# Kernel optimization log

Measured on AMD Instinct MI355X. Metric: run time of the kernel, lower is better.

The kernel has to match this reference:

```python
import jax, jax.numpy as jnp
import numpy as np

N, M, D = 100000, 50000, 256
NE = N + M
B = 131072

def kl_normal_std(mu, scale):
    # KL( N(mu, scale) || N(0, 1) ) = -log(scale) + (scale^2 + mu^2)/2 - 1/2
    return 0.5 * (scale * scale + mu * mu - 1.0) - jnp.log(scale)

def setup_inputs() -> dict:
    key = jax.random.key(0)
    ks = jax.random.split(key, 8)
    users = jax.random.randint(ks[0], (B, 1), 0, N)
    items = jax.random.randint(ks[1], (B, 1), N, NE)
    x = jnp.concatenate([users, items], axis=1)                        # [B, 2]
    bias_table = jax.random.normal(ks[2], (NE, 2), dtype=jnp.float32)
    entity_table = jax.random.normal(ks[3], (NE, 2 * D), dtype=jnp.float32)
    global_bias_mean = jnp.zeros((1,), dtype=jnp.float32)
    global_bias_scale = jnp.ones((1,), dtype=jnp.float32)
    nb_occ = jax.random.randint(ks[4], (NE,), 1, 1001)                 # train occurrence counts >= 1
    eps_bias = jax.random.normal(ks[5], (NE,), dtype=jnp.float32)
    eps_entity = jax.random.normal(ks[6], (NE, D), dtype=jnp.float32)
    eps_global = jax.random.normal(ks[7], (1,), dtype=jnp.float32)
    return {"x": x, "bias_table": bias_table, "entity_table": entity_table,
            "global_bias_mean": global_bias_mean, "global_bias_scale": global_bias_scale,
            "nb_occ": nb_occ, "eps_bias": eps_bias, "eps_entity": eps_entity,
            "eps_global": eps_global}

def reference(x, bias_table, entity_table, global_bias_mean, global_bias_scale,
              nb_occ, eps_bias, eps_entity, eps_global):
    # --- reparameterized samples (one eps per table row == one eps per unique entity) ---
    gb_scale = jnp.abs(global_bias_scale)
    global_bias = global_bias_mean + gb_scale * eps_global             # [1]

    bias_mu = bias_table[:, 0]
    bias_sc = jnp.abs(bias_table[:, 1])
    biases_all = bias_mu + bias_sc * eps_bias                          # [NE]

    ent_mu = entity_table[:, :D]
    ent_sc = jnp.abs(entity_table[:, D:])
    entities_all = ent_mu + ent_sc * eps_entity                        # [NE, D]

    # --- FM forward: bias sum + product-sum interaction ---
    pair_bias = biases_all[x].sum(axis=1)                              # [B]
    pair_emb = (entities_all[x[:, 0]] * entities_all[x[:, 1]]).sum(axis=1)  # [B]
    logits = global_bias + pair_bias + pair_emb                        # [B] (Bernoulli logits)

    # --- closed-form KL vs N(0,1), rescaled by batch/train occupancy ---
    kl_bias = kl_normal_std(bias_mu, bias_sc)                          # [NE]
    kl_entity = kl_normal_std(ent_mu, ent_sc).sum(axis=1)              # [NE]

    nb_occ_f = nb_occ.astype(jnp.float32)
    cnt = jnp.bincount(x.reshape(-1), length=NE).astype(jnp.float32)   # nb_occ_in_batch
    cnt_u = jnp.bincount(x[:, 0], length=NE).astype(jnp.float32)
    cnt_i = jnp.bincount(x[:, 1], length=NE).astype(jnp.float32)
    user_norm = (cnt_u / nb_occ_f).sum()
    item_norm = (cnt_i / nb_occ_f).sum()

    ids = jnp.arange(NE)
    scale_term = (jnp.where(ids <= N, float(N), 0.0) / user_norm
                  + jnp.where(ids > N, float(M), 0.0) / item_norm)
    kl_rescaled = ((kl_bias + kl_entity) * (cnt / nb_occ_f) * scale_term).sum()

    kl_global = kl_normal_std(global_bias_mean, gb_scale).sum()
    return logits, kl_global + kl_rescaled
```

## Files before the change

### kernel.cpp

```cpp
#include <hip/hip_runtime.h>
#include <math.h>

#define NU   100000
#define MI   50000
#define NEn  150000
#define Bp   131072

#define CB   256
#define EB   (NEn / 4)
#define TB   ((NEn + 255) / 256)
#define LB   (Bp / 8)

typedef float    f4v __attribute__((ext_vector_type(4)));
typedef _Float16 h8v __attribute__((ext_vector_type(8)));
typedef _Float16 h4v __attribute__((ext_vector_type(4)));

__device__ __forceinline__ float wred(float v) {
#pragma unroll
    for (int m = 32; m > 0; m >>= 1) v += __shfl_xor(v, m, 64);
    return v;
}
__device__ __forceinline__ float hred(float v) {
#pragma unroll
    for (int m = 16; m > 0; m >>= 1) v += __shfl_xor(v, m, 64);
    return v;
}

__global__ __launch_bounds__(256) void k_cnt_ent(
    const int4* __restrict__ x4,
    const f4v* __restrict__ et,
    const f4v* __restrict__ epse,
    const float* __restrict__ bt,
    const float* __restrict__ epsb,
    const float* __restrict__ gbm,
    const float* __restrict__ gbs,
    int*   __restrict__ cnt,
    h4v*   __restrict__ enth,
    float* __restrict__ bia,
    float* __restrict__ klpe,
    float* __restrict__ outkl)
{
    if (blockIdx.x < CB) {
        int t = blockIdx.x * 256 + threadIdx.x;
        int4 v = x4[t];
        atomicAdd(cnt + v.x, 1);
        atomicAdd(cnt + v.y, 1);
        atomicAdd(cnt + v.z, 1);
        atomicAdd(cnt + v.w, 1);
        if (t == 0) {
            float gm = gbm[0];
            float gs = fabsf(gbs[0]);
            outkl[0] = 0.5f * (gs * gs + gm * gm - 1.0f) - __logf(gs);
        }
        return;
    }

    int lane = threadIdx.x & 63;
    int e    = (blockIdx.x - CB) * 4 + (threadIdx.x >> 6);

    const f4v* row = et + (size_t)e * 128;
    f4v mu = __builtin_nontemporal_load(row + lane);
    f4v s4 = __builtin_nontemporal_load(row + 64 + lane);
    f4v ep = __builtin_nontemporal_load(epse + (size_t)e * 64 + lane);
    float scx = fabsf(s4.x), scy = fabsf(s4.y), scz = fabsf(s4.z), scw = fabsf(s4.w);

    if (enth) {
        h4v oh;
        oh.x = (_Float16)fmaf(scx, ep.x, mu.x);
        oh.y = (_Float16)fmaf(scy, ep.y, mu.y);
        oh.z = (_Float16)fmaf(scz, ep.z, mu.z);
        oh.w = (_Float16)fmaf(scw, ep.w, mu.w);
        enth[(size_t)e * 64 + lane] = oh;
    }

    float kl = 0.5f * (scx * scx + mu.x * mu.x - 1.0f) - __logf(scx)
             + 0.5f * (scy * scy + mu.y * mu.y - 1.0f) - __logf(scy)
             + 0.5f * (scz * scz + mu.z * mu.z - 1.0f) - __logf(scz)
             + 0.5f * (scw * scw + mu.w * mu.w - 1.0f) - __logf(scw);
    kl = wred(kl);

    if (lane == 0) {
        float bmu = bt[2 * e];
        float bsc = fabsf(bt[2 * e + 1]);
        bia[e]  = fmaf(bsc, epsb[e], bmu);
        klpe[e] = kl + 0.5f * (bsc * bsc + bmu * bmu - 1.0f) - __logf(bsc);
    }
}

__global__ __launch_bounds__(256) void k_log_tail(
    const int* __restrict__ x,
    const h8v* __restrict__ enth,
    const float* __restrict__ bia,
    const float* __restrict__ gbm, const float* __restrict__ gbs,
    const float* __restrict__ epsg,
    const int* __restrict__ cnt, const int* __restrict__ nb,
    const float* __restrict__ klpe,
    float* __restrict__ hdr,
    float* __restrict__ out)
{
    if (blockIdx.x < TB) {
        int e = blockIdx.x * 256 + threadIdx.x;
        float u = 0.f, i = 0.f, aa = 0.f, bb = 0.f;
        if (e < NEn) {
            float v  = (float)cnt[e] / (float)nb[e];
            float kv = klpe[e] * v;
            if (e < NU)  u  = v;  else i  = v;
            if (e <= NU) aa = kv; else bb = kv;
        }
        u = wred(u); i = wred(i); aa = wred(aa); bb = wred(bb);
        __shared__ float s[4][4];
        int wib = threadIdx.x >> 6;
        if ((threadIdx.x & 63) == 0) {
            s[wib][0] = u; s[wib][1] = i; s[wib][2] = aa; s[wib][3] = bb;
        }
        __syncthreads();
        if (threadIdx.x < 4) {
            float t = s[0][threadIdx.x] + s[1][threadIdx.x]
                    + s[2][threadIdx.x] + s[3][threadIdx.x];
            if (t != 0.f) atomicAdd(hdr + threadIdx.x, t);
        }
        return;
    }

    int lane = threadIdx.x & 63;
    int sub  = lane & 31;
    int p    = (blockIdx.x - TB) * 8 + ((threadIdx.x >> 6) << 1) + (lane >> 5);
    int u = x[2 * p], v = x[2 * p + 1];
    float bu = bia[u];
    float bv = bia[v];
    h8v a = enth[(size_t)u * 32 + sub];
    h8v b = enth[(size_t)v * 32 + sub];
    float d = 0.f;
#pragma unroll
    for (int i = 0; i < 8; ++i) d = fmaf((float)a[i], (float)b[i], d);
    d = hred(d);
    if (sub == 0) {
        float gb = fmaf(fabsf(gbs[0]), epsg[0], gbm[0]);
        __builtin_nontemporal_store(gb + bu + bv + d, out + p);
    }
}

__global__ void k_fin(const float* __restrict__ hdr, float* __restrict__ outkl) {
    if (threadIdx.x == 0)
        outkl[0] += (float)NU * hdr[2] / hdr[0] + (float)MI * hdr[3] / hdr[1];
}

__global__ __launch_bounds__(256) void k_logits_rc(
    const int* __restrict__ x, const float4* __restrict__ et,
    const float4* __restrict__ epse, const float* __restrict__ bia,
    const float* __restrict__ gbm, const float* __restrict__ gbs,
    const float* __restrict__ epsg, float* __restrict__ out)
{
    int lane = threadIdx.x & 63;
    int p    = blockIdx.x * 4 + (threadIdx.x >> 6);
    int u = x[2 * p], v = x[2 * p + 1];
    const float4* ru = et + (size_t)u * 128;
    const float4* rv = et + (size_t)v * 128;
    float4 mu_u = ru[lane], s_u = ru[64 + lane], e_u = epse[(size_t)u * 64 + lane];
    float4 mu_v = rv[lane], s_v = rv[64 + lane], e_v = epse[(size_t)v * 64 + lane];
    float ax = fmaf(fabsf(s_u.x), e_u.x, mu_u.x), bx = fmaf(fabsf(s_v.x), e_v.x, mu_v.x);
    float ay = fmaf(fabsf(s_u.y), e_u.y, mu_u.y), by = fmaf(fabsf(s_v.y), e_v.y, mu_v.y);
    float az = fmaf(fabsf(s_u.z), e_u.z, mu_u.z), bz = fmaf(fabsf(s_v.z), e_v.z, mu_v.z);
    float aw = fmaf(fabsf(s_u.w), e_u.w, mu_u.w), bw = fmaf(fabsf(s_v.w), e_v.w, mu_v.w);
    float d = ax * bx + ay * by + az * bz + aw * bw;
    d = wred(d);
    if (lane == 0) {
        float gb = fmaf(fabsf(gbs[0]), epsg[0], gbm[0]);
        out[p] = gb + bia[u] + bia[v] + d;
    }
}

extern "C" void kernel_launch(void* const* d_in, const int* in_sizes, int n_in,
                              void* d_out, int out_size, void* d_ws, size_t ws_size,
                              hipStream_t stream)
{
    const int*   x    = (const int*)d_in[0];
    const float* bt   = (const float*)d_in[1];
    const float* et   = (const float*)d_in[2];
    const float* gbm  = (const float*)d_in[3];
    const float* gbs  = (const float*)d_in[4];
    const int*   nb   = (const int*)d_in[5];
    const float* epsb = (const float*)d_in[6];
    const float* epse = (const float*)d_in[7];
    const float* epsg = (const float*)d_in[8];
    float* out = (float*)d_out;

    char*  ws   = (char*)d_ws;
    float* hdr  = (float*)ws;
    int*   cnt  = (int*)  (ws + 64);
    float* klpe = (float*)(ws + 64 + (size_t)NEn * 4);
    float* bia  = (float*)(ws + 64 + (size_t)NEn * 8);
    size_t entoff = 64 + (size_t)NEn * 12;
    h4v* enth = nullptr;
    if (ws_size >= entoff + (size_t)NEn * 512)
        enth = (h4v*)(ws + entoff);

    (void)hipMemsetAsync(ws, 0, 64 + (size_t)NEn * 4, stream);

    k_cnt_ent<<<CB + EB, 256, 0, stream>>>(
        (const int4*)x, (const f4v*)et, (const f4v*)epse, bt, epsb,
        gbm, gbs, cnt, enth, bia, klpe, out + Bp);

    if (enth) {
        k_log_tail<<<TB + LB, 256, 0, stream>>>(
            x, (const h8v*)enth, bia, gbm, gbs, epsg,
            cnt, nb, klpe, hdr, out);
    } else {
        k_log_tail<<<TB, 256, 0, stream>>>(
            x, nullptr, bia, gbm, gbs, epsg, cnt, nb, klpe, hdr, out);
        k_logits_rc<<<Bp / 4, 256, 0, stream>>>(x, (const float4*)et,
                                                (const float4*)epse, bia,
                                                gbm, gbs, epsg, out);
    }

    k_fin<<<1, 64, 0, stream>>>(hdr, out + Bp);
}
```

Before: 529.5 us.

## Replace bincount histogram with per-pair accumulation of KL weights in logits kernel

The atomic histogram pass and the memset of the count buffer are removed. Instead, the logits kernel accumulates klpe[e]/nb[e] and 1/nb[e] directly for each batch occurrence, which is algebraically the same as weighting each entity by its count. A special case sends the item index equal to N to the user-scaled sum. Both kernels become fixed-grid persistent loops, the entity kernel handles two rows per wave with vectorised bias loads, and block 0 zeroes the reduction header. The KL reduction now does scattered reads of nb and klpe per pair in exchange for dropping the histogram atomics and the separate per-entity tail pass.

```diff
diff --git a/kernel.cpp b/kernel.cpp
--- a/kernel.cpp
+++ b/kernel.cpp
@@ -6,12 +6,11 @@
 #define NEn  150000
 #define Bp   131072
 
-#define CB   256
-#define EB   (NEn / 4)
-#define TB   ((NEn + 255) / 256)
-#define LB   (Bp / 8)
+#define GRID1 2048
+#define GRID2 2048
 
 typedef float    f4v __attribute__((ext_vector_type(4)));
+typedef float    f2v __attribute__((ext_vector_type(2)));
 typedef _Float16 h8v __attribute__((ext_vector_type(8)));
 typedef _Float16 h4v __attribute__((ext_vector_type(4)));
 
@@ -26,117 +25,140 @@
     return v;
 }
 
-__global__ __launch_bounds__(256) void k_cnt_ent(
-    const int4* __restrict__ x4,
+__global__ __launch_bounds__(256) void k_ent(
     const f4v* __restrict__ et,
     const f4v* __restrict__ epse,
-    const float* __restrict__ bt,
-    const float* __restrict__ epsb,
+    const f2v* __restrict__ bt2,
+    const f2v* __restrict__ epsb2,
     const float* __restrict__ gbm,
     const float* __restrict__ gbs,
-    int*   __restrict__ cnt,
-    h4v*   __restrict__ enth,
-    float* __restrict__ bia,
-    float* __restrict__ klpe,
+    h4v*  __restrict__ enth,
+    f2v*  __restrict__ bia2,
+    f2v*  __restrict__ klpe2,
+    float* __restrict__ hdr,
     float* __restrict__ outkl)
 {
-    if (blockIdx.x < CB) {
-        int t = blockIdx.x * 256 + threadIdx.x;
-        int4 v = x4[t];
-        atomicAdd(cnt + v.x, 1);
-        atomicAdd(cnt + v.y, 1);
-        atomicAdd(cnt + v.z, 1);
-        atomicAdd(cnt + v.w, 1);
-        if (t == 0) {
-            float gm = gbm[0];
-            float gs = fabsf(gbs[0]);
+    if (blockIdx.x == 0) {
+        if (threadIdx.x < 4) hdr[threadIdx.x] = 0.f;
+        if (threadIdx.x == 0) {
+            float gm = gbm[0], gs = fabsf(gbs[0]);
             outkl[0] = 0.5f * (gs * gs + gm * gm - 1.0f) - __logf(gs);
         }
-        return;
-    }
-
-    int lane = threadIdx.x & 63;
-    int e    = (blockIdx.x - CB) * 4 + (threadIdx.x >> 6);
-
-    const f4v* row = et + (size_t)e * 128;
-    f4v mu = __builtin_nontemporal_load(row + lane);
-    f4v s4 = __builtin_nontemporal_load(row + 64 + lane);
-    f4v ep = __builtin_nontemporal_load(epse + (size_t)e * 64 + lane);
-    float scx = fabsf(s4.x), scy = fabsf(s4.y), scz = fabsf(s4.z), scw = fabsf(s4.w);
-
-    if (enth) {
-        h4v oh;
-        oh.x = (_Float16)fmaf(scx, ep.x, mu.x);
-        oh.y = (_Float16)fmaf(scy, ep.y, mu.y);
-        oh.z = (_Float16)fmaf(scz, ep.z, mu.z);
-        oh.w = (_Float16)fmaf(scw, ep.w, mu.w);
-        enth[(size_t)e * 64 + lane] = oh;
-    }
-
-    float kl = 0.5f * (scx * scx + mu.x * mu.x - 1.0f) - __logf(scx)
-             + 0.5f * (scy * scy + mu.y * mu.y - 1.0f) - __logf(scy)
-             + 0.5f * (scz * scz + mu.z * mu.z - 1.0f) - __logf(scz)
-             + 0.5f * (scw * scw + mu.w * mu.w - 1.0f) - __logf(scw);
-    kl = wred(kl);
-
-    if (lane == 0) {
-        float bmu = bt[2 * e];
-        float bsc = fabsf(bt[2 * e + 1]);
-        bia[e]  = fmaf(bsc, epsb[e], bmu);
-        klpe[e] = kl + 0.5f * (bsc * bsc + bmu * bmu - 1.0f) - __logf(bsc);
-    }
-}
-
-__global__ __launch_bounds__(256) void k_log_tail(
-    const int* __restrict__ x,
+    }
+
+    const int lane = threadIdx.x & 63;
+    const int gwav = blockIdx.x * 4 + (threadIdx.x >> 6);
+    const int step = GRID1 * 4 * 2;
+
+    for (int r0 = gwav * 2; r0 < NEn; r0 += step) {
+        const f4v* ra = et + (size_t)r0 * 128;
+        const f4v* rb = ra + 128;
+        f4v mu0 = __builtin_nontemporal_load(ra + lane);
+        f4v s40 = __builtin_nontemporal_load(ra + 64 + lane);
+        f4v mu1 = __builtin_nontemporal_load(rb + lane);
+        f4v s41 = __builtin_nontemporal_load(rb + 64 + lane);
+        f4v ep0 = __builtin_nontemporal_load(epse + (size_t)r0 * 64 + lane);
+        f4v ep1 = __builtin_nontemporal_load(epse + (size_t)r0 * 64 + 64 + lane);
+
+        float ax0 = fabsf(s40.x), ay0 = fabsf(s40.y), az0 = fabsf(s40.z), aw0 = fabsf(s40.w);
+        float ax1 = fabsf(s41.x), ay1 = fabsf(s41.y), az1 = fabsf(s41.z), aw1 = fabsf(s41.w);
+
+        if (enth) {
+            h4v o0, o1;
+            o0.x = (_Float16)fmaf(ax0, ep0.x, mu0.x);
+            o0.y = (_Float16)fmaf(ay0, ep0.y, mu0.y);
+            o0.z = (_Float16)fmaf(az0, ep0.z, mu0.z);
+            o0.w = (_Float16)fmaf(aw0, ep0.w, mu0.w);
+            o1.x = (_Float16)fmaf(ax1, ep1.x, mu1.x);
+            o1.y = (_Float16)fmaf(ay1, ep1.y, mu1.y);
+            o1.z = (_Float16)fmaf(az1, ep1.z, mu1.z);
+            o1.w = (_Float16)fmaf(aw1, ep1.w, mu1.w);
+            enth[(size_t)r0 * 64 + lane]      = o0;
+            enth[(size_t)r0 * 64 + 64 + lane] = o1;
+        }
+
+        float kl0 = 0.5f * (ax0 * ax0 + mu0.x * mu0.x - 1.0f) - __logf(ax0)
+                  + 0.5f * (ay0 * ay0 + mu0.y * mu0.y - 1.0f) - __logf(ay0)
+                  + 0.5f * (az0 * az0 + mu0.z * mu0.z - 1.0f) - __logf(az0)
+                  + 0.5f * (aw0 * aw0 + mu0.w * mu0.w - 1.0f) - __logf(aw0);
+        float kl1 = 0.5f * (ax1 * ax1 + mu1.x * mu1.x - 1.0f) - __logf(ax1)
+                  + 0.5f * (ay1 * ay1 + mu1.y * mu1.y - 1.0f) - __logf(ay1)
+                  + 0.5f * (az1 * az1 + mu1.z * mu1.z - 1.0f) - __logf(az1)
+                  + 0.5f * (aw1 * aw1 + mu1.w * mu1.w - 1.0f) - __logf(aw1);
+        kl0 = wred(kl0);
+        kl1 = wred(kl1);
+
+        if (lane == 0) {
+            f2v b0 = bt2[r0], b1 = bt2[r0 + 1];
+            f2v eb = epsb2[r0 >> 1];
+            float bs0 = fabsf(b0.y), bs1 = fabsf(b1.y);
+            f2v bo, ko;
+            bo.x = fmaf(bs0, eb.x, b0.x);
+            bo.y = fmaf(bs1, eb.y, b1.x);
+            ko.x = kl0 + 0.5f * (bs0 * bs0 + b0.x * b0.x - 1.0f) - __logf(bs0);
+            ko.y = kl1 + 0.5f * (bs1 * bs1 + b1.x * b1.x - 1.0f) - __logf(bs1);
+            bia2[r0 >> 1]  = bo;
+            klpe2[r0 >> 1] = ko;
+        }
+    }
+}
+
+__global__ __launch_bounds__(256) void k_log(
+    const int2* __restrict__ x2,
     const h8v* __restrict__ enth,
     const float* __restrict__ bia,
+    const float* __restrict__ klpe,
+    const int* __restrict__ nb,
     const float* __restrict__ gbm, const float* __restrict__ gbs,
     const float* __restrict__ epsg,
-    const int* __restrict__ cnt, const int* __restrict__ nb,
-    const float* __restrict__ klpe,
     float* __restrict__ hdr,
     float* __restrict__ out)
 {
-    if (blockIdx.x < TB) {
-        int e = blockIdx.x * 256 + threadIdx.x;
-        float u = 0.f, i = 0.f, aa = 0.f, bb = 0.f;
-        if (e < NEn) {
-            float v  = (float)cnt[e] / (float)nb[e];
-            float kv = klpe[e] * v;
-            if (e < NU)  u  = v;  else i  = v;
-            if (e <= NU) aa = kv; else bb = kv;
-        }
-        u = wred(u); i = wred(i); aa = wred(aa); bb = wred(bb);
-        __shared__ float s[4][4];
-        int wib = threadIdx.x >> 6;
-        if ((threadIdx.x & 63) == 0) {
-            s[wib][0] = u; s[wib][1] = i; s[wib][2] = aa; s[wib][3] = bb;
-        }
-        __syncthreads();
-        if (threadIdx.x < 4) {
-            float t = s[0][threadIdx.x] + s[1][threadIdx.x]
-                    + s[2][threadIdx.x] + s[3][threadIdx.x];
-            if (t != 0.f) atomicAdd(hdr + threadIdx.x, t);
-        }
-        return;
-    }
-
-    int lane = threadIdx.x & 63;
-    int sub  = lane & 31;
-    int p    = (blockIdx.x - TB) * 8 + ((threadIdx.x >> 6) << 1) + (lane >> 5);
-    int u = x[2 * p], v = x[2 * p + 1];
-    float bu = bia[u];
-    float bv = bia[v];
-    h8v a = enth[(size_t)u * 32 + sub];
-    h8v b = enth[(size_t)v * 32 + sub];
-    float d = 0.f;
+    const int lane = threadIdx.x & 63;
+    const int sub  = lane & 31;
+    const int grp  = (blockIdx.x * 4 + (threadIdx.x >> 6)) * 2 + (lane >> 5);
+    const int ngrp = GRID2 * 4 * 2;
+    const float gb = fmaf(fabsf(gbs[0]), epsg[0], gbm[0]);
+    const bool use_ent = (enth != nullptr);
+
+    float uS = 0.f, iS = 0.f, aS = 0.f, bS = 0.f;
+
+    for (int p = grp; p < Bp; p += ngrp) {
+        int2 pr = x2[p];
+        int u = pr.x, v = pr.y;
+        if (use_ent) {
+            float bu = bia[u];
+            float bv = bia[v];
+            h8v a = enth[(size_t)u * 32 + sub];
+            h8v b = enth[(size_t)v * 32 + sub];
+            float d = 0.f;
 #pragma unroll
-    for (int i = 0; i < 8; ++i) d = fmaf((float)a[i], (float)b[i], d);
-    d = hred(d);
-    if (sub == 0) {
-        float gb = fmaf(fabsf(gbs[0]), epsg[0], gbm[0]);
-        __builtin_nontemporal_store(gb + bu + bv + d, out + p);
+            for (int i = 0; i < 8; ++i) d = fmaf((float)a[i], (float)b[i], d);
+            d = hred(d);
+            if (sub == 0)
+                __builtin_nontemporal_store(gb + bu + bv + d, out + p);
+        }
+        if (sub == 0) {
+            float rnu = 1.0f / (float)nb[u];
+            float rnv = 1.0f / (float)nb[v];
+            float au  = klpe[u] * rnu;
+            float av  = klpe[v] * rnv;
+            uS += rnu;
+            iS += rnv;
+            aS += au + ((v == NU) ? av : 0.f);
+            bS += ((v > NU) ? av : 0.f);
+        }
+    }
+
+    uS = wred(uS); iS = wred(iS); aS = wred(aS); bS = wred(bS);
+    __shared__ float s[4][4];
+    int wib = threadIdx.x >> 6;
+    if (lane == 0) { s[wib][0] = uS; s[wib][1] = iS; s[wib][2] = aS; s[wib][3] = bS; }
+    __syncthreads();
+    if (threadIdx.x < 4) {
+        float t = s[0][threadIdx.x] + s[1][threadIdx.x]
+                + s[2][threadIdx.x] + s[3][threadIdx.x];
+        if (t != 0.f) atomicAdd(hdr + threadIdx.x, t);
     }
 }
 
@@ -187,31 +209,26 @@
 
     char*  ws   = (char*)d_ws;
     float* hdr  = (float*)ws;
-    int*   cnt  = (int*)  (ws + 64);
-    float* klpe = (float*)(ws + 64 + (size_t)NEn * 4);
-    float* bia  = (float*)(ws + 64 + (size_t)NEn * 8);
-    size_t entoff = 64 + (size_t)NEn * 12;
+    float* klpe = (float*)(ws + 64);
+    float* bia  = (float*)(ws + 64 + (size_t)NEn * 4);
+    size_t entoff = 64 + (size_t)NEn * 8;
     h4v* enth = nullptr;
     if (ws_size >= entoff + (size_t)NEn * 512)
         enth = (h4v*)(ws + entoff);
 
-    (void)hipMemsetAsync(ws, 0, 64 + (size_t)NEn * 4, stream);
-
-    k_cnt_ent<<<CB + EB, 256, 0, stream>>>(
-        (const int4*)x, (const f4v*)et, (const f4v*)epse, bt, epsb,
-        gbm, gbs, cnt, enth, bia, klpe, out + Bp);
-
-    if (enth) {
-        k_log_tail<<<TB + LB, 256, 0, stream>>>(
-            x, (const h8v*)enth, bia, gbm, gbs, epsg,
-            cnt, nb, klpe, hdr, out);
-    } else {
-        k_log_tail<<<TB, 256, 0, stream>>>(
-            x, nullptr, bia, gbm, gbs, epsg, cnt, nb, klpe, hdr, out);
+
+    k_ent<<<GRID1, 256, 0, stream>>>(
+        (const f4v*)et, (const f4v*)epse, (const f2v*)bt, (const f2v*)epsb,
+        gbm, gbs, enth, (f2v*)bia, (f2v*)klpe, hdr, out + Bp);
+
+    k_log<<<GRID2, 256, 0, stream>>>(
+        (const int2*)x, (const h8v*)enth, bia, klpe, nb,
+        gbm, gbs, epsg, hdr, out);
+
+    if (!enth)
         k_logits_rc<<<Bp / 4, 256, 0, stream>>>(x, (const float4*)et,
                                                 (const float4*)epse, bia,
                                                 gbm, gbs, epsg, out);
-    }
 
     k_fin<<<1, 64, 0, stream>>>(hdr, out + Bp);
 }
```

After: 554.0 us. 4.6% more time.

## Replace bincount histogram with per-pair KL accumulation and striped header atomics

Applied to the files above, without the earlier changes.

Drops the atomic histogram of entity occurrences and the per-entity tail reduction. The KL terms are now accumulated directly per pair inside the logits kernel, using the identity that a sum of cnt/nb over entities equals a sum of 1/nb over batch occurrences. This also removes the memset, since block 0 of the entity kernel zeroes the header. Header atomics are spread over 32 slots to reduce contention, and the final kernel sums them. The cost is extra random gathers of nb and klpe per pair, and a possible race because the header zeroing happens in the previous kernel.

```diff
diff --git a/kernel.cpp b/kernel.cpp
--- a/kernel.cpp
+++ b/kernel.cpp
@@ -6,11 +6,6 @@
 #define NEn  150000
 #define Bp   131072
 
-#define CB   256
-#define EB   (NEn / 4)
-#define TB   ((NEn + 255) / 256)
-#define LB   (Bp / 8)
-
 typedef float    f4v __attribute__((ext_vector_type(4)));
 typedef _Float16 h8v __attribute__((ext_vector_type(8)));
 typedef _Float16 h4v __attribute__((ext_vector_type(4)));
@@ -26,37 +21,29 @@
     return v;
 }
 
-__global__ __launch_bounds__(256) void k_cnt_ent(
-    const int4* __restrict__ x4,
+__global__ __launch_bounds__(256) void k_ent(
     const f4v* __restrict__ et,
     const f4v* __restrict__ epse,
     const float* __restrict__ bt,
     const float* __restrict__ epsb,
     const float* __restrict__ gbm,
     const float* __restrict__ gbs,
-    int*   __restrict__ cnt,
     h4v*   __restrict__ enth,
     float* __restrict__ bia,
     float* __restrict__ klpe,
+    float* __restrict__ hdr,
     float* __restrict__ outkl)
 {
-    if (blockIdx.x < CB) {
-        int t = blockIdx.x * 256 + threadIdx.x;
-        int4 v = x4[t];
-        atomicAdd(cnt + v.x, 1);
-        atomicAdd(cnt + v.y, 1);
-        atomicAdd(cnt + v.z, 1);
-        atomicAdd(cnt + v.w, 1);
-        if (t == 0) {
-            float gm = gbm[0];
-            float gs = fabsf(gbs[0]);
+    if (blockIdx.x == 0) {
+        if (threadIdx.x < 128) hdr[threadIdx.x] = 0.f;
+        if (threadIdx.x == 0) {
+            float gm = gbm[0], gs = fabsf(gbs[0]);
             outkl[0] = 0.5f * (gs * gs + gm * gm - 1.0f) - __logf(gs);
         }
-        return;
     }
 
     int lane = threadIdx.x & 63;
-    int e    = (blockIdx.x - CB) * 4 + (threadIdx.x >> 6);
+    int e    = blockIdx.x * 4 + (threadIdx.x >> 6);
 
     const f4v* row = et + (size_t)e * 128;
     f4v mu = __builtin_nontemporal_load(row + lane);
@@ -87,62 +74,76 @@
     }
 }
 
-__global__ __launch_bounds__(256) void k_log_tail(
-    const int* __restrict__ x,
+__global__ __launch_bounds__(256) void k_log(
+    const int2* __restrict__ x2,
     const h8v* __restrict__ enth,
     const float* __restrict__ bia,
+    const float* __restrict__ klpe,
+    const int* __restrict__ nb,
     const float* __restrict__ gbm, const float* __restrict__ gbs,
     const float* __restrict__ epsg,
-    const int* __restrict__ cnt, const int* __restrict__ nb,
-    const float* __restrict__ klpe,
     float* __restrict__ hdr,
     float* __restrict__ out)
 {
-    if (blockIdx.x < TB) {
-        int e = blockIdx.x * 256 + threadIdx.x;
-        float u = 0.f, i = 0.f, aa = 0.f, bb = 0.f;
-        if (e < NEn) {
-            float v  = (float)cnt[e] / (float)nb[e];
-            float kv = klpe[e] * v;
-            if (e < NU)  u  = v;  else i  = v;
-            if (e <= NU) aa = kv; else bb = kv;
+    const int lane = threadIdx.x & 63;
+    const int sub  = lane & 31;
+    const int p    = blockIdx.x * 8 + ((threadIdx.x >> 6) << 1) + (lane >> 5);
+    const bool use_ent = (enth != nullptr);
+
+    int2 pr = x2[p];
+    int u = pr.x, v = pr.y;
+
+    if (use_ent) {
+        float bu = bia[u];
+        float bv = bia[v];
+        h8v a = enth[(size_t)u * 32 + sub];
+        h8v b = enth[(size_t)v * 32 + sub];
+        float d = 0.f;
+#pragma unroll
+        for (int i = 0; i < 8; ++i) d = fmaf((float)a[i], (float)b[i], d);
+        d = hred(d);
+        if (sub == 0) {
+            float gb = fmaf(fabsf(gbs[0]), epsg[0], gbm[0]);
+            __builtin_nontemporal_store(gb + bu + bv + d, out + p);
         }
-        u = wred(u); i = wred(i); aa = wred(aa); bb = wred(bb);
-        __shared__ float s[4][4];
-        int wib = threadIdx.x >> 6;
-        if ((threadIdx.x & 63) == 0) {
-            s[wib][0] = u; s[wib][1] = i; s[wib][2] = aa; s[wib][3] = bb;
+    }
+
+    float uS = 0.f, iS = 0.f, aS = 0.f, bS = 0.f;
+    if (sub == 0) {
+        float rnu = 1.0f / (float)nb[u];
+        float rnv = 1.0f / (float)nb[v];
+        float au  = klpe[u] * rnu;
+        float av  = klpe[v] * rnv;
+        uS = rnu;
+        iS = rnv;
+        aS = au + ((v == NU) ? av : 0.f);
+        bS = ((v > NU) ? av : 0.f);
+    }
+    uS = wred(uS); iS = wred(iS); aS = wred(aS); bS = wred(bS);
+
+    __shared__ float s[4][4];
+    int wib = threadIdx.x >> 6;
+    if (lane == 0) { s[wib][0] = uS; s[wib][1] = iS; s[wib][2] = aS; s[wib][3] = bS; }
+    __syncthreads();
+    if (threadIdx.x < 4) {
+        float t = s[0][threadIdx.x] + s[1][threadIdx.x]
+                + s[2][threadIdx.x] + s[3][threadIdx.x];
+        atomicAdd(hdr + (blockIdx.x & 31) * 4 + threadIdx.x, t);
+    }
+}
+
+__global__ void k_fin(const float* __restrict__ hdr, float* __restrict__ outkl) {
+    if (threadIdx.x == 0) {
+        float U = 0.f, I = 0.f, A = 0.f, Bv = 0.f;
+#pragma unroll
+        for (int i = 0; i < 32; ++i) {
+            U  += hdr[i * 4 + 0];
+            I  += hdr[i * 4 + 1];
+            A  += hdr[i * 4 + 2];
+            Bv += hdr[i * 4 + 3];
         }
-        __syncthreads();
-        if (threadIdx.x < 4) {
-            float t = s[0][threadIdx.x] + s[1][threadIdx.x]
-                    + s[2][threadIdx.x] + s[3][threadIdx.x];
-            if (t != 0.f) atomicAdd(hdr + threadIdx.x, t);
-        }
-        return;
-    }
-
-    int lane = threadIdx.x & 63;
-    int sub  = lane & 31;
-    int p    = (blockIdx.x - TB) * 8 + ((threadIdx.x >> 6) << 1) + (lane >> 5);
-    int u = x[2 * p], v = x[2 * p + 1];
-    float bu = bia[u];
-    float bv = bia[v];
-    h8v a = enth[(size_t)u * 32 + sub];
-    h8v b = enth[(size_t)v * 32 + sub];
-    float d = 0.f;
-#pragma unroll
-    for (int i = 0; i < 8; ++i) d = fmaf((float)a[i], (float)b[i], d);
-    d = hred(d);
-    if (sub == 0) {
-        float gb = fmaf(fabsf(gbs[0]), epsg[0], gbm[0]);
-        __builtin_nontemporal_store(gb + bu + bv + d, out + p);
-    }
-}
-
-__global__ void k_fin(const float* __restrict__ hdr, float* __restrict__ outkl) {
-    if (threadIdx.x == 0)
-        outkl[0] += (float)NU * hdr[2] / hdr[0] + (float)MI * hdr[3] / hdr[1];
+        outkl[0] += (float)NU * A / U + (float)MI * Bv / I;
+    }
 }
 
 __global__ __launch_bounds__(256) void k_logits_rc(
@@ -187,31 +188,26 @@
 
     char*  ws   = (char*)d_ws;
     float* hdr  = (float*)ws;
-    int*   cnt  = (int*)  (ws + 64);
-    float* klpe = (float*)(ws + 64 + (size_t)NEn * 4);
-    float* bia  = (float*)(ws + 64 + (size_t)NEn * 8);
-    size_t entoff = 64 + (size_t)NEn * 12;
+    float* klpe = (float*)(ws + 512);
+    float* bia  = (float*)(ws + 512 + (size_t)NEn * 4);
+    size_t entoff = 512 + (size_t)NEn * 8;
     h4v* enth = nullptr;
     if (ws_size >= entoff + (size_t)NEn * 512)
         enth = (h4v*)(ws + entoff);
 
-    (void)hipMemsetAsync(ws, 0, 64 + (size_t)NEn * 4, stream);
-
-    k_cnt_ent<<<CB + EB, 256, 0, stream>>>(
-        (const int4*)x, (const f4v*)et, (const f4v*)epse, bt, epsb,
-        gbm, gbs, cnt, enth, bia, klpe, out + Bp);
-
-    if (enth) {
-        k_log_tail<<<TB + LB, 256, 0, stream>>>(
-            x, (const h8v*)enth, bia, gbm, gbs, epsg,
-            cnt, nb, klpe, hdr, out);
-    } else {
-        k_log_tail<<<TB, 256, 0, stream>>>(
-            x, nullptr, bia, gbm, gbs, epsg, cnt, nb, klpe, hdr, out);
+
+    k_ent<<<NEn / 4, 256, 0, stream>>>(
+        (const f4v*)et, (const f4v*)epse, bt, epsb,
+        gbm, gbs, enth, bia, klpe, hdr, out + Bp);
+
+    k_log<<<Bp / 8, 256, 0, stream>>>(
+        (const int2*)x, (const h8v*)enth, bia, klpe, nb,
+        gbm, gbs, epsg, hdr, out);
+
+    if (!enth)
         k_logits_rc<<<Bp / 4, 256, 0, stream>>>(x, (const float4*)et,
                                                 (const float4*)epse, bia,
                                                 gbm, gbs, epsg, out);
-    }
 
     k_fin<<<1, 64, 0, stream>>>(hdr, out + Bp);
 }
```

After: 550.3 us. 1.04x slower.
